# Kernel optimization log

Hardware: AMD Instinct MI355X
Metric: run time of the kernel (lower is better)

Reference implementation:

```python
import jax, jax.numpy as jnp
import numpy as np

B, IN_CH, D, H, W = 2, 4, 8, 224, 224
DS = 4
DIM, HEADS, HEAD_DIM, LAYERS = 256, 8, 32, 4
INNER = HEADS * HEAD_DIM
MLP = 4 * DIM
WS = (4, 8, 8)
SHIFT = (2, 4, 4)
WVOL = WS[0] * WS[1] * WS[2]
Hp, Wp = H // DS, W // DS
NW = (D // WS[0]) * (Hp // WS[1]) * (Wp // WS[2])
NBIAS = (2 * WS[0] - 1) * (2 * WS[1] - 1) * (2 * WS[2] - 1)


def _rel_index():
    c = np.stack(np.meshgrid(np.arange(WS[0]), np.arange(WS[1]), np.arange(WS[2]), indexing='ij')).reshape(3, -1)
    r = (c[:, :, None] - c[:, None, :]).transpose(1, 2, 0)
    r[..., 0] += WS[0] - 1
    r[..., 1] += WS[1] - 1
    r[..., 2] += WS[2] - 1
    return r[..., 0] * (2 * WS[1] - 1) * (2 * WS[2] - 1) + r[..., 1] * (2 * WS[2] - 1) + r[..., 2]

REL_IDX = jnp.asarray(_rel_index())  # (WVOL, WVOL)


def _shift_mask():
    # standard Swin shifted-window attention mask on the post-merge grid
    img = np.zeros((D, Hp, Wp), np.int32)
    cnt = 0
    sl = lambda w, s: (slice(0, -w), slice(-w, -s), slice(-s, None))
    for sd in sl(WS[0], SHIFT[0]):
        for sh in sl(WS[1], SHIFT[1]):
            for sw in sl(WS[2], SHIFT[2]):
                img[sd, sh, sw] = cnt
                cnt += 1
    m = img.reshape(D // WS[0], WS[0], Hp // WS[1], WS[1], Wp // WS[2], WS[2])
    m = m.transpose(0, 2, 4, 1, 3, 5).reshape(NW, WVOL)
    return jnp.asarray(np.where(m[:, None, :] != m[:, :, None], -1e9, 0.0).astype(np.float32))

ATTN_MASK = _shift_mask()  # (NW, WVOL, WVOL)


def layer_norm(x, s, b):
    mu = x.mean(-1, keepdims=True)
    var = x.var(-1, keepdims=True)
    return (x - mu) / jnp.sqrt(var + 1e-5) * s + b


def window_attention(x, qkv_w, out_w, out_b, bias_tab, shifted):
    # x: (B, D, Hp, Wp, C) channel-last
    if shifted:
        x = jnp.roll(x, (-SHIFT[0], -SHIFT[1], -SHIFT[2]), axis=(1, 2, 3))
    xw = x.reshape(B, D // WS[0], WS[0], Hp // WS[1], WS[1], Wp // WS[2], WS[2], DIM)
    xw = xw.transpose(0, 1, 3, 5, 2, 4, 6, 7).reshape(B, NW, WVOL, DIM)
    qkv = xw @ qkv_w  # (B, NW, WVOL, 3*INNER)
    q, k, v = jnp.split(qkv, 3, axis=-1)
    split = lambda t: t.reshape(B, NW, WVOL, HEADS, HEAD_DIM).transpose(0, 1, 3, 2, 4)
    q = split(q) * (HEAD_DIM ** -0.5)
    k, v = split(k), split(v)
    attn = jnp.einsum('bwhid,bwhjd->bwhij', q, k)  # (B, NW, H, WVOL, WVOL)
    bias = bias_tab[REL_IDX].transpose(2, 0, 1)  # (H, WVOL, WVOL)
    attn = attn + bias
    if shifted:
        attn = attn + ATTN_MASK[None, :, None]
    attn = jax.nn.softmax(attn, axis=-1)
    o = jnp.einsum('bwhij,bwhjd->bwhid', attn, v)
    o = o.transpose(0, 1, 3, 2, 4).reshape(B, NW, WVOL, INNER)
    o = o @ out_w + out_b
    o = o.reshape(B, D // WS[0], Hp // WS[1], Wp // WS[2], WS[0], WS[1], WS[2], DIM)
    o = o.transpose(0, 1, 4, 2, 5, 3, 6, 7).reshape(B, D, Hp, Wp, DIM)
    if shifted:
        o = jnp.roll(o, SHIFT, axis=(1, 2, 3))
    return o


def setup_inputs() -> dict:
    key = jax.random.key(0)
    ks = jax.random.split(key, 12)
    s = 0.02
    return {
        'x': jax.random.normal(ks[0], (B, IN_CH, D, H, W), jnp.float32),
        'conv_w': jax.random.normal(ks[1], (DIM, IN_CH, 1, DS, DS), jnp.float32) * s,
        'conv_b': jnp.zeros((DIM,), jnp.float32),
        'ln1_s': jnp.ones((LAYERS, DIM), jnp.float32),
        'ln1_b': jnp.zeros((LAYERS, DIM), jnp.float32),
        'qkv_w': jax.random.normal(ks[2], (LAYERS, DIM, 3 * INNER), jnp.float32) * s,
        'out_w': jax.random.normal(ks[3], (LAYERS, INNER, DIM), jnp.float32) * s,
        'out_b': jnp.zeros((LAYERS, DIM), jnp.float32),
        'bias_tab': jax.random.normal(ks[4], (LAYERS, NBIAS, HEADS), jnp.float32) * s,
        'ln2_s': jnp.ones((LAYERS, DIM), jnp.float32),
        'ln2_b': jnp.zeros((LAYERS, DIM), jnp.float32),
        'fc1_w': jax.random.normal(ks[5], (LAYERS, DIM, MLP), jnp.float32) * s,
        'fc1_b': jnp.zeros((LAYERS, MLP), jnp.float32),
        'fc2_w': jax.random.normal(ks[6], (LAYERS, MLP, DIM), jnp.float32) * s,
        'fc2_b': jnp.zeros((LAYERS, DIM), jnp.float32),
    }


def reference(x, conv_w, conv_b, ln1_s, ln1_b, qkv_w, out_w, out_b, bias_tab, ln2_s, ln2_b, fc1_w, fc1_b, fc2_w, fc2_b):
    # patch merge: Conv3d kernel (1, DS, DS) stride (1, DS, DS)
    y = jax.lax.conv_general_dilated(
        x, conv_w, window_strides=(1, DS, DS), padding='VALID',
        dimension_numbers=('NCDHW', 'OIDHW', 'NCDHW'))
    y = y + conv_b[None, :, None, None, None]
    y = y.transpose(0, 2, 3, 4, 1)  # (B, D, Hp, Wp, DIM) channel-last
    for i in range(LAYERS):
        shifted = (i % 2 == 1)
        y = y + window_attention(layer_norm(y, ln1_s[i], ln1_b[i]),
                                 qkv_w[i], out_w[i], out_b[i], bias_tab[i], shifted)
        h = layer_norm(y, ln2_s[i], ln2_b[i])
        h = jax.nn.gelu(h @ fc1_w[i] + fc1_b[i]) @ fc2_w[i] + fc2_b[i]
        y = y + h
    return y.transpose(0, 4, 1, 2, 3)  # (B, DIM, D, Hp, Wp)
```

## Files before the change

kernel.cpp:

```cpp
#include <hip/hip_runtime.h>

typedef unsigned short ushort_t;
typedef unsigned int   uint_t;

#define NTOK 50176
#define NWIN 98
#define NBIAS 1575

typedef __attribute__((ext_vector_type(8))) short bf16x8;
typedef __attribute__((ext_vector_type(4))) float floatx4;

static __device__ __forceinline__ float lo2f(uint_t u) { return __uint_as_float(u << 16); }
static __device__ __forceinline__ float hi2f(uint_t u) { return __uint_as_float(u & 0xffff0000u); }
static __device__ __forceinline__ ushort_t f2b(float f) {
    union { float f; uint_t u; } v; v.f = f;
    uint_t u = v.u + 0x7fffu + ((v.u >> 16) & 1u);
    return (ushort_t)(u >> 16);
}

__global__ void transpose_w(const float* __restrict__ src, ushort_t* __restrict__ dst,
                            int K, int N) {
    long base = (long)blockIdx.y * K * N;
    int idx = blockIdx.x * 256 + threadIdx.x;
    if (idx < K * N) {
        int k = idx / N, n = idx - k * N;
        dst[base + (long)n * K + k] = f2b(src[base + idx]);
    }
}

__global__ void cast_bf16(const float* __restrict__ src, ushort_t* __restrict__ dst, int n) {
    int i = blockIdx.x * 256 + threadIdx.x;
    if (i < n) dst[i] = f2b(src[i]);
}

__global__ void im2row(const float* __restrict__ X, ushort_t* __restrict__ A) {
    int idx = blockIdx.x * 256 + threadIdx.x;
    int t = idx >> 4;
    int k = idx & 15;
    int ic = k >> 2, kh = k & 3;
    int w = t % 56, h = (t / 56) % 56, d = (t / 3136) % 8, b = t / 25088;
    long xi = (((long)(b * 4 + ic) * 8 + d) * 224 + (h * 4 + kh)) * 224 + w * 4;
    float4 u = *(const float4*)(X + xi);
    ushort_t* ap = A + (long)t * 64 + ic * 16 + kh * 4;
    ap[0] = f2b(u.x); ap[1] = f2b(u.y); ap[2] = f2b(u.z); ap[3] = f2b(u.w);
}

__global__ void ln_kernel(const float* __restrict__ Y, ushort_t* __restrict__ Xn,
                          const float* __restrict__ S, const float* __restrict__ Bb) {
    int wv = threadIdx.x >> 6, lane = threadIdx.x & 63;
    long t = (long)blockIdx.x * 4 + wv;
    const float* y = Y + t * 256;
    float v[4], s = 0.f, s2 = 0.f;
#pragma unroll
    for (int r = 0; r < 4; ++r) { v[r] = y[lane + 64 * r]; s += v[r]; s2 += v[r] * v[r]; }
#pragma unroll
    for (int off = 32; off; off >>= 1) { s += __shfl_xor(s, off, 64); s2 += __shfl_xor(s2, off, 64); }
    float mu = s * (1.f / 256.f);
    float var = s2 * (1.f / 256.f) - mu * mu;
    float rstd = rsqrtf(var + 1e-5f);
#pragma unroll
    for (int r = 0; r < 4; ++r) {
        int c = lane + 64 * r;
        Xn[t * 256 + c] = f2b((v[r] - mu) * rstd * S[c] + Bb[c]);
    }
}

__global__ __launch_bounds__(256, 2) void gemm_bt(
    const ushort_t* __restrict__ A, const ushort_t* __restrict__ BT,
    int M, int N, int K,
    const float* __restrict__ bias, int mode,
    ushort_t* __restrict__ C, float* __restrict__ Y) {
    __shared__ ushort_t As[128 * 32];
    __shared__ ushort_t Bs[128 * 32];
    const int tid = threadIdx.x;
    const int wv = tid >> 6;
    const int lane = tid & 63;
    const int quad = lane >> 4;
    const int l15 = lane & 15;
    const long m0 = (long)blockIdx.x * 128;
    const long n0 = (long)blockIdx.y * 128;
    const int wm = (wv & 1) * 64;
    const int wn = (wv >> 1) * 64;
    const int r_loc = lane >> 2;
    const int k_loc = (lane & 3) * 8;

    floatx4 acc[4][4] = {};

    const ushort_t* Ab = A + m0 * K;
    const ushort_t* Bb = BT + n0 * K;

    for (int kt = 0; kt < K; kt += 32) {
#pragma unroll
        for (int q = 0; q < 2; ++q) {
            int slot = wv * 2 + q;
            int row = slot * 16 + r_loc;
            __builtin_amdgcn_global_load_lds(
                (const __attribute__((address_space(1))) void*)(Ab + (long)row * K + kt + k_loc),
                (__attribute__((address_space(3))) void*)(As + slot * 512), 16, 0, 0);
            __builtin_amdgcn_global_load_lds(
                (const __attribute__((address_space(1))) void*)(Bb + (long)row * K + kt + k_loc),
                (__attribute__((address_space(3))) void*)(Bs + slot * 512), 16, 0, 0);
        }
        __syncthreads();
        bf16x8 af[4], bfr[4];
#pragma unroll
        for (int i = 0; i < 4; ++i) {
            af[i]  = *(const bf16x8*)(As + (wm + i * 16 + l15) * 32 + quad * 8);
            bfr[i] = *(const bf16x8*)(Bs + (wn + i * 16 + l15) * 32 + quad * 8);
        }
#pragma unroll
        for (int mi = 0; mi < 4; ++mi)
#pragma unroll
            for (int ni = 0; ni < 4; ++ni)
                acc[mi][ni] = __builtin_amdgcn_mfma_f32_16x16x32_bf16(af[mi], bfr[ni], acc[mi][ni], 0, 0, 0);
        __syncthreads();
    }

    if (mode == 2) {
#pragma unroll
        for (int mi = 0; mi < 4; ++mi)
#pragma unroll
            for (int ni = 0; ni < 4; ++ni) {
                long col = n0 + wn + ni * 16 + l15;
                float bv = bias[col];
#pragma unroll
                for (int r = 0; r < 4; ++r) {
                    long row = m0 + wm + mi * 16 + quad * 4 + r;
                    Y[row * N + col] += acc[mi][ni][r] + bv;
                }
            }
    } else if (mode == 3) {
#pragma unroll
        for (int mi = 0; mi < 4; ++mi)
#pragma unroll
            for (int ni = 0; ni < 4; ++ni) {
                long col = n0 + wn + ni * 16 + l15;
                float bv = bias[col];
#pragma unroll
                for (int r = 0; r < 4; ++r) {
                    long row = m0 + wm + mi * 16 + quad * 4 + r;
                    Y[row * N + col] = acc[mi][ni][r] + bv;
                }
            }
    } else {
#pragma unroll
        for (int mi = 0; mi < 4; ++mi)
#pragma unroll
            for (int ni = 0; ni < 4; ++ni) {
                long col = n0 + wn + ni * 16 + l15;
                float bv = bias ? bias[col] : 0.f;
#pragma unroll
                for (int r = 0; r < 4; ++r) {
                    long row = m0 + wm + mi * 16 + quad * 4 + r;
                    float v = acc[mi][ni][r] + bv;
                    if (mode == 1) {
                        float x3 = v * v * v;
                        v = 0.5f * v * (1.f + tanhf(0.7978845608028654f * (v + 0.044715f * x3)));
                    }
                    C[row * N + col] = f2b(v);
                }
            }
    }
}

#define PSTRIDE 260
#define VTSTRIDE 264
__global__ __launch_bounds__(256, 2) void attn_mfma(
    const ushort_t* __restrict__ QKV, ushort_t* __restrict__ O,
    const float* __restrict__ BiasTab, int shifted) {
    __shared__ ushort_t Ks[256 * 32];
    __shared__ ushort_t Vt[32 * VTSTRIDE];
    __shared__ ushort_t Pl[4 * 16 * PSTRIDE];
    __shared__ float bias_s[NBIAS];
    __shared__ int tok_s[256];
    __shared__ int reg_s[256];

    const int tid = threadIdx.x;
    const int wv = tid >> 6;
    const int lane = tid & 63;
    const int quad = lane >> 4;
    const int l15 = lane & 15;
    const int wdx = blockIdx.x, hd = blockIdx.y, b = blockIdx.z;
    const int wd = wdx / 49;
    const int wh = (wdx / 7) % 7;
    const int ww = wdx % 7;

    {
        const int t = tid;
        const int di = t >> 6, hi = (t >> 3) & 7, wi = t & 7;
        const int d = wd * 4 + di, h = wh * 8 + hi, w = ww * 8 + wi;
        int d0 = d, h0 = h, w0 = w;
        if (shifted) { d0 = (d + 2) & 7; h0 = (h + 4) % 56; w0 = (w + 4) % 56; }
        const long tok = ((long)((b * 8 + d0) * 56 + h0)) * 56 + w0;
        tok_s[t] = (int)tok;
        if (shifted) {
            int rd = d < 4 ? 0 : (d < 6 ? 1 : 2);
            int rh = h < 48 ? 0 : (h < 52 ? 1 : 2);
            int rw = w < 48 ? 0 : (w < 52 ? 1 : 2);
            reg_s[t] = rd * 9 + rh * 3 + rw;
        } else reg_s[t] = 0;
        const uint4* kp = (const uint4*)(QKV + tok * 768 + 256 + hd * 32);
        const uint4* vp = (const uint4*)(QKV + tok * 768 + 512 + hd * 32);
        uint4* kd = (uint4*)(Ks + t * 32);
#pragma unroll
        for (int p = 0; p < 4; ++p) kd[p] = kp[p];
#pragma unroll
        for (int p = 0; p < 4; ++p) {
            uint4 vvu = vp[p];
            uint_t uu[4] = {vvu.x, vvu.y, vvu.z, vvu.w};
#pragma unroll
            for (int e = 0; e < 4; ++e) {
                int dd = p * 8 + e * 2;
                Vt[dd * VTSTRIDE + t]       = (ushort_t)(uu[e] & 0xffffu);
                Vt[(dd + 1) * VTSTRIDE + t] = (ushort_t)(uu[e] >> 16);
            }
        }
        for (int r = t; r < NBIAS; r += 256) bias_s[r] = BiasTab[r * 8 + hd];
    }
    __syncthreads();

    const float scale = 0.17677669529663687f;
    ushort_t* Pw = Pl + wv * 16 * PSTRIDE;

    for (int rg = 0; rg < 4; ++rg) {
        const int rti = wv * 4 + rg;
        bf16x8 aq;
        {
            int tq = tok_s[rti * 16 + l15];
            const uint4* qp = (const uint4*)(QKV + (long)tq * 768 + hd * 32 + quad * 8);
            union { uint4 u; bf16x8 v; } cv; cv.u = *qp; aq = cv.v;
        }
        int idv[4], ihv[4], iwv4[4], rq[4];
#pragma unroll
        for (int r = 0; r < 4; ++r) {
            int i = rti * 16 + quad * 4 + r;
            idv[r] = i >> 6; ihv[r] = (i >> 3) & 7; iwv4[r] = i & 7;
            rq[r] = reg_s[i];
        }
        floatx4 Sc[16];
#pragma unroll
        for (int nt = 0; nt < 16; ++nt) {
            bf16x8 bk = *(const bf16x8*)(Ks + (nt * 16 + l15) * 32 + quad * 8);
            floatx4 z = {};
            Sc[nt] = __builtin_amdgcn_mfma_f32_16x16x32_bf16(aq, bk, z, 0, 0, 0);
        }
        float m4[4] = {-3e38f, -3e38f, -3e38f, -3e38f};
#pragma unroll
        for (int nt = 0; nt < 16; ++nt) {
            int j = nt * 16 + l15;
            int jd = j >> 6, jh = (j >> 3) & 7, jw = j & 7;
            int rk = reg_s[j];
#pragma unroll
            for (int r = 0; r < 4; ++r) {
                float s = Sc[nt][r] * scale +
                          bias_s[(idv[r] - jd + 3) * 225 + (ihv[r] - jh + 7) * 15 + (iwv4[r] - jw + 7)];
                if (shifted && (rq[r] != rk)) s = -1e9f;
                Sc[nt][r] = s;
                m4[r] = fmaxf(m4[r], s);
            }
        }
#pragma unroll
        for (int r = 0; r < 4; ++r) {
            m4[r] = fmaxf(m4[r], __shfl_xor(m4[r], 1));
            m4[r] = fmaxf(m4[r], __shfl_xor(m4[r], 2));
            m4[r] = fmaxf(m4[r], __shfl_xor(m4[r], 4));
            m4[r] = fmaxf(m4[r], __shfl_xor(m4[r], 8));
        }
        float l4[4] = {0.f, 0.f, 0.f, 0.f};
#pragma unroll
        for (int nt = 0; nt < 16; ++nt)
#pragma unroll
            for (int r = 0; r < 4; ++r) {
                float p = __expf(Sc[nt][r] - m4[r]);
                l4[r] += p;
                Sc[nt][r] = p;
            }
#pragma unroll
        for (int r = 0; r < 4; ++r) {
            l4[r] += __shfl_xor(l4[r], 1);
            l4[r] += __shfl_xor(l4[r], 2);
            l4[r] += __shfl_xor(l4[r], 4);
            l4[r] += __shfl_xor(l4[r], 8);
        }
#pragma unroll
        for (int nt = 0; nt < 16; ++nt)
#pragma unroll
            for (int r = 0; r < 4; ++r)
                Pw[(quad * 4 + r) * PSTRIDE + nt * 16 + l15] = f2b(Sc[nt][r]);
        __builtin_amdgcn_s_waitcnt(0xC07F);
        __builtin_amdgcn_wave_barrier();
        float inv4[4];
#pragma unroll
        for (int r = 0; r < 4; ++r) inv4[r] = 1.f / l4[r];
#pragma unroll
        for (int ct = 0; ct < 2; ++ct) {
            floatx4 oa = {};
#pragma unroll
            for (int kt = 0; kt < 8; ++kt) {
                bf16x8 ap = *(const bf16x8*)(Pw + l15 * PSTRIDE + kt * 32 + quad * 8);
                bf16x8 bv = *(const bf16x8*)(Vt + (ct * 16 + l15) * VTSTRIDE + kt * 32 + quad * 8);
                oa = __builtin_amdgcn_mfma_f32_16x16x32_bf16(ap, bv, oa, 0, 0, 0);
            }
#pragma unroll
            for (int r = 0; r < 4; ++r) {
                int i = rti * 16 + quad * 4 + r;
                long tq = tok_s[i];
                O[tq * 256 + hd * 32 + ct * 16 + l15] = f2b(oa[r] * inv4[r]);
            }
        }
        __builtin_amdgcn_s_waitcnt(0xC07F);
        __builtin_amdgcn_wave_barrier();
    }
}

__global__ void out_permute(const float* __restrict__ Y, float* __restrict__ Out) {
    __shared__ float tile[64][65];
    const int t0 = blockIdx.x * 64;
    const int c0 = blockIdx.y * 64;
    const int tid = threadIdx.x;
    const int a = tid >> 6;
    const int bx = tid & 63;
#pragma unroll
    for (int s8 = 0; s8 < 16; ++s8) {
        int tt = a + s8 * 4;
        tile[tt][bx] = Y[(long)(t0 + tt) * 256 + c0 + bx];
    }
    __syncthreads();
#pragma unroll
    for (int s8 = 0; s8 < 16; ++s8) {
        int cc = a + s8 * 4;
        int tok = t0 + bx;
        int bb = tok / 25088;
        int rem = tok - bb * 25088;
        Out[((long)(bb * 256 + c0 + cc)) * 25088 + rem] = tile[bx][cc];
    }
}

extern "C" void kernel_launch(void* const* d_in, const int* in_sizes, int n_in,
                              void* d_out, int out_size, void* d_ws, size_t ws_size,
                              hipStream_t stream) {
    (void)in_sizes; (void)n_in; (void)out_size; (void)ws_size;
    const float* x        = (const float*)d_in[0];
    const float* conv_w   = (const float*)d_in[1];
    const float* conv_b   = (const float*)d_in[2];
    const float* ln1_s    = (const float*)d_in[3];
    const float* ln1_b    = (const float*)d_in[4];
    const float* qkv_w    = (const float*)d_in[5];
    const float* out_w    = (const float*)d_in[6];
    const float* out_b    = (const float*)d_in[7];
    const float* bias_tab = (const float*)d_in[8];
    const float* ln2_s    = (const float*)d_in[9];
    const float* ln2_b    = (const float*)d_in[10];
    const float* fc1_w    = (const float*)d_in[11];
    const float* fc1_b    = (const float*)d_in[12];
    const float* fc2_w    = (const float*)d_in[13];
    const float* fc2_b    = (const float*)d_in[14];
    float* out = (float*)d_out;

    char* ws = (char*)d_ws;
    float*    y    = (float*)ws;    ws += (size_t)NTOK * 256 * 4;
    ushort_t* big  = (ushort_t*)ws; ws += (size_t)NTOK * 1024 * 2;
    ushort_t* xob  = (ushort_t*)ws; ws += (size_t)NTOK * 256 * 2;
    ushort_t* bt_qkv = (ushort_t*)ws; ws += (size_t)4 * 768 * 256 * 2;
    ushort_t* bt_out = (ushort_t*)ws; ws += (size_t)4 * 256 * 256 * 2;
    ushort_t* bt_fc1 = (ushort_t*)ws; ws += (size_t)4 * 1024 * 256 * 2;
    ushort_t* bt_fc2 = (ushort_t*)ws; ws += (size_t)4 * 256 * 1024 * 2;
    ushort_t* cw_bf  = (ushort_t*)ws; ws += (size_t)256 * 64 * 2;

    transpose_w<<<dim3((256 * 768 + 255) / 256, 4), 256, 0, stream>>>(qkv_w, bt_qkv, 256, 768);
    transpose_w<<<dim3((256 * 256 + 255) / 256, 4), 256, 0, stream>>>(out_w, bt_out, 256, 256);
    transpose_w<<<dim3((256 * 1024 + 255) / 256, 4), 256, 0, stream>>>(fc1_w, bt_fc1, 256, 1024);
    transpose_w<<<dim3((1024 * 256 + 255) / 256, 4), 256, 0, stream>>>(fc2_w, bt_fc2, 1024, 256);

    cast_bf16<<<(256 * 64 + 255) / 256, 256, 0, stream>>>(conv_w, cw_bf, 256 * 64);
    im2row<<<NTOK * 16 / 256, 256, 0, stream>>>(x, big);
    gemm_bt<<<dim3(NTOK / 128, 2), 256, 0, stream>>>(
        big, cw_bf, NTOK, 256, 64, conv_b, 3, nullptr, y);

    for (int i = 0; i < 4; ++i) {
        int sh = i & 1;
        ln_kernel<<<NTOK / 4, 256, 0, stream>>>(y, xob, ln1_s + i * 256, ln1_b + i * 256);
        gemm_bt<<<dim3(NTOK / 128, 6), 256, 0, stream>>>(
            xob, bt_qkv + (size_t)i * 768 * 256, NTOK, 768, 256, nullptr, 0, big, nullptr);
        attn_mfma<<<dim3(NWIN, 8, 2), 256, 0, stream>>>(
            big, xob, bias_tab + (size_t)i * NBIAS * 8, sh);
        gemm_bt<<<dim3(NTOK / 128, 2), 256, 0, stream>>>(
            xob, bt_out + (size_t)i * 256 * 256, NTOK, 256, 256, out_b + i * 256, 2, nullptr, y);
        ln_kernel<<<NTOK / 4, 256, 0, stream>>>(y, xob, ln2_s + i * 256, ln2_b + i * 256);
        gemm_bt<<<dim3(NTOK / 128, 8), 256, 0, stream>>>(
            xob, bt_fc1 + (size_t)i * 1024 * 256, NTOK, 1024, 256, fc1_b + i * 1024, 1, big, nullptr);
        gemm_bt<<<dim3(NTOK / 128, 2), 256, 0, stream>>>(
            big, bt_fc2 + (size_t)i * 256 * 1024, NTOK, 256, 1024, fc2_b + i * 256, 2, nullptr, y);
    }

    out_permute<<<dim3(NTOK / 64, 4), 256, 0, stream>>>(y, out);
}
```

Baseline: 1.454 ms.

## Store QKV in window-major per-head layout and streamline attention softmax

The QKV GEMM epilogue now scatters outputs into a head-major, window-ordered layout (with the cyclic shift folded in). Attention therefore reads contiguous per-window Q/K/V and writes window-ordered output, and the out-projection GEMM maps window tokens back to image tokens while accumulating into the residual. The relative position bias is pre-expanded once into a dense per-layer, per-head 256x256 table, which replaces the per-element index math. Attention computes S transposed so the softmax probabilities feed the PV MFMA straight from registers without the LDS staging buffer. It also loads K with global_load_lds, skips masking for unshifted windows, and raises occupancy to 4 blocks. In exchange it adds an extra 8 MB bias buffer, scattered epilogue stores in the GEMMs, and strided bias reads from global memory.

```diff
diff --git a/kernel.cpp b/kernel.cpp
--- a/kernel.cpp
+++ b/kernel.cpp
@@ -16,6 +16,24 @@
     union { float f; uint_t u; } v; v.f = f;
     uint_t u = v.u + 0x7fffu + ((v.u >> 16) & 1u);
     return (ushort_t)(u >> 16);
+}
+
+static __device__ __forceinline__ int tok2wtok(int t, int sh) {
+    int b = t / 25088, rem = t - b * 25088;
+    int d = rem / 3136, r1 = rem - d * 3136;
+    int h = r1 / 56, w = r1 - h * 56;
+    if (sh) { d = (d + 6) & 7; h -= 4; if (h < 0) h += 56; w -= 4; if (w < 0) w += 56; }
+    return ((b * 98 + (d >> 2) * 49 + (h >> 3) * 7 + (w >> 3)) << 8) |
+           ((d & 3) << 6) | ((h & 7) << 3) | (w & 7);
+}
+static __device__ __forceinline__ int wtok2tok(int wt, int sh) {
+    int b = wt / 25088, rem = wt - b * 25088;
+    int win = rem >> 8, pos = rem & 255;
+    int wd = win / 49, r1 = win - wd * 49;
+    int wh = r1 / 7, ww = r1 - wh * 7;
+    int d = wd * 4 + (pos >> 6), h = wh * 8 + ((pos >> 3) & 7), w = ww * 8 + (pos & 7);
+    if (sh) { d = (d + 2) & 7; h += 4; if (h >= 56) h -= 56; w += 4; if (w >= 56) w -= 56; }
+    return (b * 8 + d) * 3136 + h * 56 + w;
 }
 
 __global__ void transpose_w(const float* __restrict__ src, ushort_t* __restrict__ dst,
@@ -31,6 +49,16 @@
 __global__ void cast_bf16(const float* __restrict__ src, ushort_t* __restrict__ dst, int n) {
     int i = blockIdx.x * 256 + threadIdx.x;
     if (i < n) dst[i] = f2b(src[i]);
+}
+
+__global__ void expand_bias(const float* __restrict__ bias_tab, float* __restrict__ Bx) {
+    int j = blockIdx.x, hd = blockIdx.y, l = blockIdx.z;
+    int i = threadIdx.x;
+    int rd = (i >> 6) - (j >> 6) + 3;
+    int rh = ((i >> 3) & 7) - ((j >> 3) & 7) + 7;
+    int rw = (i & 7) - (j & 7) + 7;
+    int idx = rd * 225 + rh * 15 + rw;
+    Bx[((((size_t)l * 8 + hd) << 8) + j) * 256 + i] = bias_tab[((size_t)l * NBIAS + idx) * 8 + hd];
 }
 
 __global__ void im2row(const float* __restrict__ X, ushort_t* __restrict__ A) {
@@ -69,7 +97,7 @@
     const ushort_t* __restrict__ A, const ushort_t* __restrict__ BT,
     int M, int N, int K,
     const float* __restrict__ bias, int mode,
-    ushort_t* __restrict__ C, float* __restrict__ Y) {
+    ushort_t* __restrict__ C, float* __restrict__ Y, int sh) {
     __shared__ ushort_t As[128 * 32];
     __shared__ ushort_t Bs[128 * 32];
     const int tid = threadIdx.x;
@@ -142,6 +170,39 @@
                     Y[row * N + col] = acc[mi][ni][r] + bv;
                 }
             }
+    } else if (mode == 4) {
+#pragma unroll
+        for (int mi = 0; mi < 4; ++mi) {
+            int wt[4];
+#pragma unroll
+            for (int r = 0; r < 4; ++r)
+                wt[r] = tok2wtok((int)(m0 + wm + mi * 16 + quad * 4 + r), sh);
+#pragma unroll
+            for (int ni = 0; ni < 4; ++ni) {
+                int c = (int)(n0 + wn + ni * 16 + l15);
+                int mat = c >> 8, hh = (c >> 5) & 7, ch = c & 31;
+                size_t pb = ((size_t)(mat * 8 + hh) * NTOK) * 32 + ch;
+#pragma unroll
+                for (int r = 0; r < 4; ++r)
+                    C[pb + (size_t)wt[r] * 32] = f2b(acc[mi][ni][r]);
+            }
+        }
+    } else if (mode == 5) {
+#pragma unroll
+        for (int mi = 0; mi < 4; ++mi) {
+            int tk[4];
+#pragma unroll
+            for (int r = 0; r < 4; ++r)
+                tk[r] = wtok2tok((int)(m0 + wm + mi * 16 + quad * 4 + r), sh);
+#pragma unroll
+            for (int ni = 0; ni < 4; ++ni) {
+                long col = n0 + wn + ni * 16 + l15;
+                float bv = bias[col];
+#pragma unroll
+                for (int r = 0; r < 4; ++r)
+                    Y[(size_t)tk[r] * N + col] += acc[mi][ni][r] + bv;
+            }
+        }
     } else {
 #pragma unroll
         for (int mi = 0; mi < 4; ++mi)
@@ -163,16 +224,12 @@
     }
 }
 
-#define PSTRIDE 260
-#define VTSTRIDE 264
-__global__ __launch_bounds__(256, 2) void attn_mfma(
+#define VTS 268
+__global__ __launch_bounds__(256, 4) void attn_mfma(
     const ushort_t* __restrict__ QKV, ushort_t* __restrict__ O,
-    const float* __restrict__ BiasTab, int shifted) {
+    const float* __restrict__ Bx, int shifted) {
     __shared__ ushort_t Ks[256 * 32];
-    __shared__ ushort_t Vt[32 * VTSTRIDE];
-    __shared__ ushort_t Pl[4 * 16 * PSTRIDE];
-    __shared__ float bias_s[NBIAS];
-    __shared__ int tok_s[256];
+    __shared__ ushort_t Vt[32 * VTS];
     __shared__ int reg_s[256];
 
     const int tid = threadIdx.x;
@@ -180,136 +237,121 @@
     const int lane = tid & 63;
     const int quad = lane >> 4;
     const int l15 = lane & 15;
-    const int wdx = blockIdx.x, hd = blockIdx.y, b = blockIdx.z;
-    const int wd = wdx / 49;
-    const int wh = (wdx / 7) % 7;
-    const int ww = wdx % 7;
+    const int win = blockIdx.x, hd = blockIdx.y, b = blockIdx.z;
+    const int wd = win / 49, r1w = win - wd * 49;
+    const int wh = r1w / 7, ww = r1w - wh * 7;
+    const size_t wbase = ((size_t)b * 98 + win) * 256;
+    const ushort_t* Qg = QKV + ((size_t)hd * NTOK + wbase) * 32;
+    const ushort_t* Kg = QKV + ((size_t)(8 + hd) * NTOK + wbase) * 32;
+    const ushort_t* Vg = QKV + ((size_t)(16 + hd) * NTOK + wbase) * 32;
 
     {
-        const int t = tid;
-        const int di = t >> 6, hi = (t >> 3) & 7, wi = t & 7;
-        const int d = wd * 4 + di, h = wh * 8 + hi, w = ww * 8 + wi;
-        int d0 = d, h0 = h, w0 = w;
-        if (shifted) { d0 = (d + 2) & 7; h0 = (h + 4) % 56; w0 = (w + 4) % 56; }
-        const long tok = ((long)((b * 8 + d0) * 56 + h0)) * 56 + w0;
-        tok_s[t] = (int)tok;
-        if (shifted) {
-            int rd = d < 4 ? 0 : (d < 6 ? 1 : 2);
-            int rh = h < 48 ? 0 : (h < 52 ? 1 : 2);
-            int rw = w < 48 ? 0 : (w < 52 ? 1 : 2);
-            reg_s[t] = rd * 9 + rh * 3 + rw;
-        } else reg_s[t] = 0;
-        const uint4* kp = (const uint4*)(QKV + tok * 768 + 256 + hd * 32);
-        const uint4* vp = (const uint4*)(QKV + tok * 768 + 512 + hd * 32);
-        uint4* kd = (uint4*)(Ks + t * 32);
-#pragma unroll
-        for (int p = 0; p < 4; ++p) kd[p] = kp[p];
+        int pos = tid;
+        int d = wd * 4 + (pos >> 6), h = wh * 8 + ((pos >> 3) & 7), w = ww * 8 + (pos & 7);
+        int rd = d < 4 ? 0 : (d < 6 ? 1 : 2);
+        int rh = h < 48 ? 0 : (h < 52 ? 1 : 2);
+        int rw = w < 48 ? 0 : (w < 52 ? 1 : 2);
+        reg_s[pos] = rd * 9 + rh * 3 + rw;
+    }
+    {
+#pragma unroll
+        for (int q = 0; q < 4; ++q) {
+            int off = wv * 2048 + q * 512;
+            __builtin_amdgcn_global_load_lds(
+                (const __attribute__((address_space(1))) void*)(Kg + off + lane * 8),
+                (__attribute__((address_space(3))) void*)(Ks + off), 16, 0, 0);
+        }
+        const uint4* vsrc = (const uint4*)Vg;
 #pragma unroll
         for (int p = 0; p < 4; ++p) {
-            uint4 vvu = vp[p];
-            uint_t uu[4] = {vvu.x, vvu.y, vvu.z, vvu.w};
+            int u = tid + p * 256;
+            uint4 vv = vsrc[u];
+            int tok = u >> 2, chb = (u & 3) * 8;
+            uint_t uu[4] = {vv.x, vv.y, vv.z, vv.w};
 #pragma unroll
             for (int e = 0; e < 4; ++e) {
-                int dd = p * 8 + e * 2;
-                Vt[dd * VTSTRIDE + t]       = (ushort_t)(uu[e] & 0xffffu);
-                Vt[(dd + 1) * VTSTRIDE + t] = (ushort_t)(uu[e] >> 16);
-            }
-        }
-        for (int r = t; r < NBIAS; r += 256) bias_s[r] = BiasTab[r * 8 + hd];
+                Vt[(chb + 2 * e) * VTS + tok]     = (ushort_t)(uu[e] & 0xffffu);
+                Vt[(chb + 2 * e + 1) * VTS + tok] = (ushort_t)(uu[e] >> 16);
+            }
+        }
     }
     __syncthreads();
 
+    const int hm = shifted && (wd == 1 || wh == 6 || ww == 6);
     const float scale = 0.17677669529663687f;
-    ushort_t* Pw = Pl + wv * 16 * PSTRIDE;
+    const float* bb = Bx + ((size_t)hd << 16) + l15;
 
     for (int rg = 0; rg < 4; ++rg) {
-        const int rti = wv * 4 + rg;
-        bf16x8 aq;
-        {
-            int tq = tok_s[rti * 16 + l15];
-            const uint4* qp = (const uint4*)(QKV + (long)tq * 768 + hd * 32 + quad * 8);
-            union { uint4 u; bf16x8 v; } cv; cv.u = *qp; aq = cv.v;
-        }
-        int idv[4], ihv[4], iwv4[4], rq[4];
-#pragma unroll
-        for (int r = 0; r < 4; ++r) {
-            int i = rti * 16 + quad * 4 + r;
-            idv[r] = i >> 6; ihv[r] = (i >> 3) & 7; iwv4[r] = i & 7;
-            rq[r] = reg_s[i];
-        }
+        const int q0 = (wv * 4 + rg) * 16;
+        bf16x8 aq = *(const bf16x8*)(Qg + (size_t)(q0 + l15) * 32 + quad * 8);
         floatx4 Sc[16];
 #pragma unroll
         for (int nt = 0; nt < 16; ++nt) {
             bf16x8 bk = *(const bf16x8*)(Ks + (nt * 16 + l15) * 32 + quad * 8);
             floatx4 z = {};
-            Sc[nt] = __builtin_amdgcn_mfma_f32_16x16x32_bf16(aq, bk, z, 0, 0, 0);
-        }
-        float m4[4] = {-3e38f, -3e38f, -3e38f, -3e38f};
-#pragma unroll
-        for (int nt = 0; nt < 16; ++nt) {
-            int j = nt * 16 + l15;
-            int jd = j >> 6, jh = (j >> 3) & 7, jw = j & 7;
-            int rk = reg_s[j];
+            Sc[nt] = __builtin_amdgcn_mfma_f32_16x16x32_bf16(bk, aq, z, 0, 0, 0);
+        }
+        float mx = -3e38f;
+        const float* bq = bb + q0;
+        if (!hm) {
+#pragma unroll
+            for (int nt = 0; nt < 16; ++nt)
+#pragma unroll
+                for (int r = 0; r < 4; ++r) {
+                    float s = fmaf(Sc[nt][r], scale, bq[(nt * 16 + quad * 4 + r) << 8]);
+                    Sc[nt][r] = s; mx = fmaxf(mx, s);
+                }
+        } else {
+            int myreg = reg_s[q0 + l15];
+#pragma unroll
+            for (int nt = 0; nt < 16; ++nt)
+#pragma unroll
+                for (int r = 0; r < 4; ++r) {
+                    int key = nt * 16 + quad * 4 + r;
+                    float s = fmaf(Sc[nt][r], scale, bq[key << 8]);
+                    s = (reg_s[key] == myreg) ? s : -1e9f;
+                    Sc[nt][r] = s; mx = fmaxf(mx, s);
+                }
+        }
+        mx = fmaxf(mx, __shfl_xor(mx, 16, 64));
+        mx = fmaxf(mx, __shfl_xor(mx, 32, 64));
+        float lsum = 0.f;
+#pragma unroll
+        for (int nt = 0; nt < 16; ++nt)
 #pragma unroll
             for (int r = 0; r < 4; ++r) {
-                float s = Sc[nt][r] * scale +
-                          bias_s[(idv[r] - jd + 3) * 225 + (ihv[r] - jh + 7) * 15 + (iwv4[r] - jw + 7)];
-                if (shifted && (rq[r] != rk)) s = -1e9f;
-                Sc[nt][r] = s;
-                m4[r] = fmaxf(m4[r], s);
-            }
-        }
-#pragma unroll
-        for (int r = 0; r < 4; ++r) {
-            m4[r] = fmaxf(m4[r], __shfl_xor(m4[r], 1));
-            m4[r] = fmaxf(m4[r], __shfl_xor(m4[r], 2));
-            m4[r] = fmaxf(m4[r], __shfl_xor(m4[r], 4));
-            m4[r] = fmaxf(m4[r], __shfl_xor(m4[r], 8));
-        }
-        float l4[4] = {0.f, 0.f, 0.f, 0.f};
-#pragma unroll
-        for (int nt = 0; nt < 16; ++nt)
-#pragma unroll
-            for (int r = 0; r < 4; ++r) {
-                float p = __expf(Sc[nt][r] - m4[r]);
-                l4[r] += p;
-                Sc[nt][r] = p;
-            }
-#pragma unroll
-        for (int r = 0; r < 4; ++r) {
-            l4[r] += __shfl_xor(l4[r], 1);
-            l4[r] += __shfl_xor(l4[r], 2);
-            l4[r] += __shfl_xor(l4[r], 4);
-            l4[r] += __shfl_xor(l4[r], 8);
-        }
-#pragma unroll
-        for (int nt = 0; nt < 16; ++nt)
-#pragma unroll
-            for (int r = 0; r < 4; ++r)
-                Pw[(quad * 4 + r) * PSTRIDE + nt * 16 + l15] = f2b(Sc[nt][r]);
-        __builtin_amdgcn_s_waitcnt(0xC07F);
-        __builtin_amdgcn_wave_barrier();
-        float inv4[4];
-#pragma unroll
-        for (int r = 0; r < 4; ++r) inv4[r] = 1.f / l4[r];
+                float p = __expf(Sc[nt][r] - mx);
+                lsum += p; Sc[nt][r] = p;
+            }
+        lsum += __shfl_xor(lsum, 16, 64);
+        lsum += __shfl_xor(lsum, 32, 64);
+        float inv = 1.f / lsum;
+        floatx4 oc[2] = {{0.f,0.f,0.f,0.f},{0.f,0.f,0.f,0.f}};
+        const ushort_t* vr = Vt + quad * 4;
+#pragma unroll
+        for (int kt = 0; kt < 8; ++kt) {
+            union { uint_t u[4]; bf16x8 v; } bp;
+            bp.u[0] = __builtin_amdgcn_perm(__float_as_uint(Sc[2*kt][1]),   __float_as_uint(Sc[2*kt][0]),   0x07060302u);
+            bp.u[1] = __builtin_amdgcn_perm(__float_as_uint(Sc[2*kt][3]),   __float_as_uint(Sc[2*kt][2]),   0x07060302u);
+            bp.u[2] = __builtin_amdgcn_perm(__float_as_uint(Sc[2*kt+1][1]), __float_as_uint(Sc[2*kt+1][0]), 0x07060302u);
+            bp.u[3] = __builtin_amdgcn_perm(__float_as_uint(Sc[2*kt+1][3]), __float_as_uint(Sc[2*kt+1][2]), 0x07060302u);
+#pragma unroll
+            for (int ct = 0; ct < 2; ++ct) {
+                const ushort_t* vrow = vr + (ct * 16 + l15) * VTS;
+                union { unsigned long long l[2]; bf16x8 v; } av;
+                av.l[0] = *(const unsigned long long*)(vrow + 2 * kt * 16);
+                av.l[1] = *(const unsigned long long*)(vrow + 2 * kt * 16 + 16);
+                oc[ct] = __builtin_amdgcn_mfma_f32_16x16x32_bf16(av.v, bp.v, oc[ct], 0, 0, 0);
+            }
+        }
+        size_t obase = (wbase + q0 + l15) * 256 + hd * 32 + quad * 4;
 #pragma unroll
         for (int ct = 0; ct < 2; ++ct) {
-            floatx4 oa = {};
-#pragma unroll
-            for (int kt = 0; kt < 8; ++kt) {
-                bf16x8 ap = *(const bf16x8*)(Pw + l15 * PSTRIDE + kt * 32 + quad * 8);
-                bf16x8 bv = *(const bf16x8*)(Vt + (ct * 16 + l15) * VTSTRIDE + kt * 32 + quad * 8);
-                oa = __builtin_amdgcn_mfma_f32_16x16x32_bf16(ap, bv, oa, 0, 0, 0);
-            }
-#pragma unroll
-            for (int r = 0; r < 4; ++r) {
-                int i = rti * 16 + quad * 4 + r;
-                long tq = tok_s[i];
-                O[tq * 256 + hd * 32 + ct * 16 + l15] = f2b(oa[r] * inv4[r]);
-            }
-        }
-        __builtin_amdgcn_s_waitcnt(0xC07F);
-        __builtin_amdgcn_wave_barrier();
+            uint2 st;
+            st.x = (uint_t)f2b(oc[ct][0] * inv) | ((uint_t)f2b(oc[ct][1] * inv) << 16);
+            st.y = (uint_t)f2b(oc[ct][2] * inv) | ((uint_t)f2b(oc[ct][3] * inv) << 16);
+            *(uint2*)(O + obase + ct * 16) = st;
+        }
     }
 }
 
@@ -366,31 +408,33 @@
     ushort_t* bt_fc1 = (ushort_t*)ws; ws += (size_t)4 * 1024 * 256 * 2;
     ushort_t* bt_fc2 = (ushort_t*)ws; ws += (size_t)4 * 256 * 1024 * 2;
     ushort_t* cw_bf  = (ushort_t*)ws; ws += (size_t)256 * 64 * 2;
+    float*    Bx     = (float*)ws;  ws += (size_t)4 * 8 * 256 * 256 * 4;
 
     transpose_w<<<dim3((256 * 768 + 255) / 256, 4), 256, 0, stream>>>(qkv_w, bt_qkv, 256, 768);
     transpose_w<<<dim3((256 * 256 + 255) / 256, 4), 256, 0, stream>>>(out_w, bt_out, 256, 256);
     transpose_w<<<dim3((256 * 1024 + 255) / 256, 4), 256, 0, stream>>>(fc1_w, bt_fc1, 256, 1024);
     transpose_w<<<dim3((1024 * 256 + 255) / 256, 4), 256, 0, stream>>>(fc2_w, bt_fc2, 1024, 256);
+    expand_bias<<<dim3(256, 8, 4), 256, 0, stream>>>(bias_tab, Bx);
 
     cast_bf16<<<(256 * 64 + 255) / 256, 256, 0, stream>>>(conv_w, cw_bf, 256 * 64);
     im2row<<<NTOK * 16 / 256, 256, 0, stream>>>(x, big);
     gemm_bt<<<dim3(NTOK / 128, 2), 256, 0, stream>>>(
-        big, cw_bf, NTOK, 256, 64, conv_b, 3, nullptr, y);
+        big, cw_bf, NTOK, 256, 64, conv_b, 3, nullptr, y, 0);
 
     for (int i = 0; i < 4; ++i) {
         int sh = i & 1;
         ln_kernel<<<NTOK / 4, 256, 0, stream>>>(y, xob, ln1_s + i * 256, ln1_b + i * 256);
         gemm_bt<<<dim3(NTOK / 128, 6), 256, 0, stream>>>(
-            xob, bt_qkv + (size_t)i * 768 * 256, NTOK, 768, 256, nullptr, 0, big, nullptr);
+            xob, bt_qkv + (size_t)i * 768 * 256, NTOK, 768, 256, nullptr, 4, big, nullptr, sh);
         attn_mfma<<<dim3(NWIN, 8, 2), 256, 0, stream>>>(
-            big, xob, bias_tab + (size_t)i * NBIAS * 8, sh);
+            big, xob, Bx + (size_t)i * 8 * 65536, sh);
         gemm_bt<<<dim3(NTOK / 128, 2), 256, 0, stream>>>(
-            xob, bt_out + (size_t)i * 256 * 256, NTOK, 256, 256, out_b + i * 256, 2, nullptr, y);
+            xob, bt_out + (size_t)i * 256 * 256, NTOK, 256, 256, out_b + i * 256, 5, nullptr, y, sh);
         ln_kernel<<<NTOK / 4, 256, 0, stream>>>(y, xob, ln2_s + i * 256, ln2_b + i * 256);
         gemm_bt<<<dim3(NTOK / 128, 8), 256, 0, stream>>>(
-            xob, bt_fc1 + (size_t)i * 1024 * 256, NTOK, 1024, 256, fc1_b + i * 1024, 1, big, nullptr);
+            xob, bt_fc1 + (size_t)i * 1024 * 256, NTOK, 1024, 256, fc1_b + i * 1024, 1, big, nullptr, 0);
         gemm_bt<<<dim3(NTOK / 128, 2), 256, 0, stream>>>(
-            big, bt_fc2 + (size_t)i * 256 * 1024, NTOK, 256, 1024, fc2_b + i * 256, 2, nullptr, y);
+            big, bt_fc2 + (size_t)i * 256 * 1024, NTOK, 256, 1024, fc2_b + i * 256, 2, nullptr, y, 0);
     }
 
     out_permute<<<dim3(NTOK / 64, 4), 256, 0, stream>>>(y, out);
```

New measurement: 2.344 ms. 61.2% more time.
